# Performance work log

Measured on AMD Instinct MI355X. Metric: run time of the kernel, lower is better.

Reference implementation:

```python
import jax, jax.numpy as jnp
import numpy as np


def setup_inputs() -> dict:
    key = jax.random.key(0)
    k1, k2, k3 = jax.random.split(key, 3)
    B, T, D = 8, 4096, 1024
    x0 = jax.random.normal(k1, (B, D), dtype=jnp.float32)
    a = jax.random.uniform(k2, (B, T, D), dtype=jnp.float32)  # decay in [0,1) for stability
    u = jax.random.normal(k3, (B, T, D), dtype=jnp.float32)
    return {"x0": x0, "a": a, "u": u}


def _linear_scan(x0, a, u):
    # x_t = a_t * x_{t-1} + u_t, t = 1..T (x_0 given)
    # Fold x0 into the first step so the associative scan handles it uniformly.
    u0 = u.at[:, 0, :].add(a[:, 0, :] * x0)

    def combine(c1, c2):
        a1, u1 = c1
        a2, u2 = c2
        return a1 * a2, a2 * u1 + u2

    _, x = jax.lax.associative_scan(combine, (a, u0), axis=1)
    return x  # [B, T, D]


def reference(x0, a, u):
    return _linear_scan(x0, a, u)
```

## Files before the change

### kernel.cpp

```cpp
#include <hip/hip_runtime.h>

#define BB 8
#define TT 4096
#define DD 1024
#define SS 128
#define TSEG (TT / SS)

__global__ __launch_bounds__(256) void seg_reduce(
    const float* __restrict__ a, const float* __restrict__ u,
    float* __restrict__ wsA, float* __restrict__ wsU) {
  const int blk = blockIdx.x;
  const int b = blk / SS;
  const int s = blk % SS;
  const int d4 = threadIdx.x * 4;

  const size_t base = ((size_t)b * TT + (size_t)s * TSEG) * DD + d4;
  const float4* __restrict__ ap = (const float4*)(a + base);
  const float4* __restrict__ up = (const float4*)(u + base);

  float4 A = make_float4(1.f, 1.f, 1.f, 1.f);
  float4 U = make_float4(0.f, 0.f, 0.f, 0.f);

#pragma unroll 8
  for (int t = 0; t < TSEG; ++t) {
    const float4 av = ap[(size_t)t * (DD / 4)];
    const float4 uv = up[(size_t)t * (DD / 4)];
    U.x = fmaf(av.x, U.x, uv.x);
    U.y = fmaf(av.y, U.y, uv.y);
    U.z = fmaf(av.z, U.z, uv.z);
    U.w = fmaf(av.w, U.w, uv.w);
    A.x *= av.x;
    A.y *= av.y;
    A.z *= av.z;
    A.w *= av.w;
  }

  const size_t w = ((size_t)b * SS + s) * DD + d4;
  *(float4*)(wsA + w) = A;
  *(float4*)(wsU + w) = U;
}

__global__ __launch_bounds__(256) void seg_scan(
    const float* __restrict__ x0, const float* __restrict__ wsA,
    const float* __restrict__ wsU, float* __restrict__ xstart) {
  const int tid = blockIdx.x * 256 + threadIdx.x;
  const int b = tid / DD;
  const int d = tid % DD;

  float x = x0[(size_t)b * DD + d];
  size_t idx = ((size_t)b * SS) * DD + d;
#pragma unroll 4
  for (int s = 0; s < SS; ++s) {
    xstart[idx] = x;
    x = fmaf(wsA[idx], x, wsU[idx]);
    idx += DD;
  }
}

__global__ __launch_bounds__(256) void seg_apply(
    const float* __restrict__ a, const float* __restrict__ u,
    const float* __restrict__ xstart, float* __restrict__ out) {
  const int blk = blockIdx.x;
  const int b = blk / SS;
  const int s = blk % SS;
  const int d4 = threadIdx.x * 4;

  const size_t base = ((size_t)b * TT + (size_t)s * TSEG) * DD + d4;
  const float4* __restrict__ ap = (const float4*)(a + base);
  const float4* __restrict__ up = (const float4*)(u + base);
  float4* __restrict__ op = (float4*)(out + base);

  const size_t w = ((size_t)b * SS + s) * DD + d4;
  float4 x = *(const float4*)(xstart + w);

#pragma unroll 8
  for (int t = 0; t < TSEG; ++t) {
    const float4 av = ap[(size_t)t * (DD / 4)];
    const float4 uv = up[(size_t)t * (DD / 4)];
    x.x = fmaf(av.x, x.x, uv.x);
    x.y = fmaf(av.y, x.y, uv.y);
    x.z = fmaf(av.z, x.z, uv.z);
    x.w = fmaf(av.w, x.w, uv.w);
    op[(size_t)t * (DD / 4)] = x;
  }
}

extern "C" void kernel_launch(void* const* d_in, const int* in_sizes, int n_in,
                              void* d_out, int out_size, void* d_ws, size_t ws_size,
                              hipStream_t stream) {
  const float* x0 = (const float*)d_in[0];
  const float* a  = (const float*)d_in[1];
  const float* u  = (const float*)d_in[2];
  float* out = (float*)d_out;

  const size_t seg_elems = (size_t)BB * SS * DD;
  float* wsA    = (float*)d_ws;
  float* wsU    = wsA + seg_elems;
  float* xstart = wsU + seg_elems;

  seg_reduce<<<BB * SS, 256, 0, stream>>>(a, u, wsA, wsU);
  seg_scan<<<(BB * DD) / 256, 256, 0, stream>>>(x0, wsA, wsU, xstart);
  seg_apply<<<BB * SS, 256, 0, stream>>>(a, u, xstart, out);
}
```

Measured before the change: 388.4 us.

## Parallelize segment scan across waves via LDS and add register prefetch

The middle scan kernel now stages a 64-channel slab of segment summaries in shared memory. Four waves each scan a quarter of the segments, then combine the wave totals to find their starting state. This replaces one long serial global-memory chain per thread with shorter chains. The reduce and apply kernels also gain explicit two-ahead software prefetch with a lower unroll factor, which adds redundant clamped loads at the tail.

```diff
diff --git a/kernel.cpp b/kernel.cpp
--- a/kernel.cpp
+++ b/kernel.cpp
@@ -5,14 +5,23 @@
 #define DD 1024
 #define SS 128
 #define TSEG (TT / SS)
+#define STR (DD / 4)
+
+static __device__ __forceinline__ float4 ffma4(const float4 a, const float4 x,
+                                               const float4 u) {
+  return make_float4(fmaf(a.x, x.x, u.x), fmaf(a.y, x.y, u.y),
+                     fmaf(a.z, x.z, u.z), fmaf(a.w, x.w, u.w));
+}
+static __device__ __forceinline__ float4 fmul4(const float4 a, const float4 b) {
+  return make_float4(a.x * b.x, a.y * b.y, a.z * b.z, a.w * b.w);
+}
 
 __global__ __launch_bounds__(256) void seg_reduce(
     const float* __restrict__ a, const float* __restrict__ u,
     float* __restrict__ wsA, float* __restrict__ wsU) {
-  const int blk = blockIdx.x;
-  const int b = blk / SS;
-  const int s = blk % SS;
-  const int d4 = threadIdx.x * 4;
+  const int b = blockIdx.x >> 7;
+  const int s = blockIdx.x & (SS - 1);
+  const int d4 = threadIdx.x << 2;
 
   const size_t base = ((size_t)b * TT + (size_t)s * TSEG) * DD + d4;
   const float4* __restrict__ ap = (const float4*)(a + base);
@@ -21,18 +30,18 @@
   float4 A = make_float4(1.f, 1.f, 1.f, 1.f);
   float4 U = make_float4(0.f, 0.f, 0.f, 0.f);
 
-#pragma unroll 8
+  float4 ac = ap[0], uc = up[0];
+  float4 an = ap[STR], un = up[STR];
+
+#pragma unroll 4
   for (int t = 0; t < TSEG; ++t) {
-    const float4 av = ap[(size_t)t * (DD / 4)];
-    const float4 uv = up[(size_t)t * (DD / 4)];
-    U.x = fmaf(av.x, U.x, uv.x);
-    U.y = fmaf(av.y, U.y, uv.y);
-    U.z = fmaf(av.z, U.z, uv.z);
-    U.w = fmaf(av.w, U.w, uv.w);
-    A.x *= av.x;
-    A.y *= av.y;
-    A.z *= av.z;
-    A.w *= av.w;
+    const float4 av = ac, uv = uc;
+    ac = an; uc = un;
+    const int tn = (t + 2 < TSEG) ? (t + 2) : (TSEG - 1);
+    an = ap[(size_t)tn * STR];
+    un = up[(size_t)tn * STR];
+    U = ffma4(av, U, uv);
+    A = fmul4(A, av);
   }
 
   const size_t w = ((size_t)b * SS + s) * DD + d4;
@@ -43,27 +52,56 @@
 __global__ __launch_bounds__(256) void seg_scan(
     const float* __restrict__ x0, const float* __restrict__ wsA,
     const float* __restrict__ wsU, float* __restrict__ xstart) {
-  const int tid = blockIdx.x * 256 + threadIdx.x;
-  const int b = tid / DD;
-  const int d = tid % DD;
+  __shared__ float ldsA[SS * 64];
+  __shared__ float ldsU[SS * 64];
+  __shared__ float wsumA[4][64];
+  __shared__ float wsumU[4][64];
 
-  float x = x0[(size_t)b * DD + d];
-  size_t idx = ((size_t)b * SS) * DD + d;
-#pragma unroll 4
-  for (int s = 0; s < SS; ++s) {
-    xstart[idx] = x;
-    x = fmaf(wsA[idx], x, wsU[idx]);
-    idx += DD;
+  const int b  = blockIdx.x >> 4;
+  const int d0 = (blockIdx.x & 15) << 6;
+  const int ch = threadIdx.x & 63;
+  const int wv = threadIdx.x >> 6;
+
+#pragma unroll 8
+  for (int it = 0; it < SS / 4; ++it) {
+    const int s = (it << 2) + wv;
+    const size_t g = ((size_t)b * SS + s) * DD + d0 + ch;
+    ldsA[s * 64 + ch] = wsA[g];
+    ldsU[s * 64 + ch] = wsU[g];
+  }
+  __syncthreads();
+
+  float Ac = 1.f, Uc = 0.f;
+  const int s0 = wv * (SS / 4);
+#pragma unroll 8
+  for (int k = 0; k < SS / 4; ++k) {
+    const float As = ldsA[(s0 + k) * 64 + ch];
+    const float Us = ldsU[(s0 + k) * 64 + ch];
+    Uc = fmaf(As, Uc, Us);
+    Ac *= As;
+  }
+  wsumA[wv][ch] = Ac;
+  wsumU[wv][ch] = Uc;
+  __syncthreads();
+
+  float x = x0[(size_t)b * DD + d0 + ch];
+  for (int w2 = 0; w2 < wv; ++w2)
+    x = fmaf(wsumA[w2][ch], x, wsumU[w2][ch]);
+
+#pragma unroll 8
+  for (int k = 0; k < SS / 4; ++k) {
+    const int s = s0 + k;
+    xstart[((size_t)b * SS + s) * DD + d0 + ch] = x;
+    x = fmaf(ldsA[s * 64 + ch], x, ldsU[s * 64 + ch]);
   }
 }
 
 __global__ __launch_bounds__(256) void seg_apply(
     const float* __restrict__ a, const float* __restrict__ u,
     const float* __restrict__ xstart, float* __restrict__ out) {
-  const int blk = blockIdx.x;
-  const int b = blk / SS;
-  const int s = blk % SS;
-  const int d4 = threadIdx.x * 4;
+  const int b = blockIdx.x >> 7;
+  const int s = blockIdx.x & (SS - 1);
+  const int d4 = threadIdx.x << 2;
 
   const size_t base = ((size_t)b * TT + (size_t)s * TSEG) * DD + d4;
   const float4* __restrict__ ap = (const float4*)(a + base);
@@ -73,15 +111,18 @@
   const size_t w = ((size_t)b * SS + s) * DD + d4;
   float4 x = *(const float4*)(xstart + w);
 
-#pragma unroll 8
+  float4 ac = ap[0], uc = up[0];
+  float4 an = ap[STR], un = up[STR];
+
+#pragma unroll 4
   for (int t = 0; t < TSEG; ++t) {
-    const float4 av = ap[(size_t)t * (DD / 4)];
-    const float4 uv = up[(size_t)t * (DD / 4)];
-    x.x = fmaf(av.x, x.x, uv.x);
-    x.y = fmaf(av.y, x.y, uv.y);
-    x.z = fmaf(av.z, x.z, uv.z);
-    x.w = fmaf(av.w, x.w, uv.w);
-    op[(size_t)t * (DD / 4)] = x;
+    const float4 av = ac, uv = uc;
+    ac = an; uc = un;
+    const int tn = (t + 2 < TSEG) ? (t + 2) : (TSEG - 1);
+    an = ap[(size_t)tn * STR];
+    un = up[(size_t)tn * STR];
+    x = ffma4(av, x, uv);
+    op[(size_t)t * STR] = x;
   }
 }
 
@@ -99,6 +140,6 @@
   float* xstart = wsU + seg_elems;
 
   seg_reduce<<<BB * SS, 256, 0, stream>>>(a, u, wsA, wsU);
-  seg_scan<<<(BB * DD) / 256, 256, 0, stream>>>(x0, wsA, wsU, xstart);
+  seg_scan<<<BB * (DD / 64), 256, 0, stream>>>(x0, wsA, wsU, xstart);
   seg_apply<<<BB * SS, 256, 0, stream>>>(a, u, xstart, out);
 }
```

Result: faster. 378.2 us (-2.6%).
